# Kernel tuning notes

Hardware: AMD Instinct MI355X
Metric: run time of the kernel (lower is better)

Reference implementation:

```python
import jax, jax.numpy as jnp
import numpy as np

MARGIN = 0.3
N_CLASSES = 1024
N_SAMPLES = 32
D = 512


def setup_inputs() -> dict:
    key = jax.random.key(0)
    k1, k2 = jax.random.split(key)
    embeddings = jax.random.normal(k1, (2 * N_CLASSES * N_SAMPLES, D), dtype=jnp.float32)
    target = jax.random.randint(k2, (2 * N_CLASSES * N_SAMPLES,), 0, N_CLASSES, dtype=jnp.int64)
    return {"embeddings": embeddings, "target": target}


def reference(embeddings, target):
    # [C, 2, S, D]: per class, block 0 = positives, block 1 = negatives
    e = embeddings.reshape(N_CLASSES, 2, N_SAMPLES, D)
    pos = e[:, 0]  # [C, S, D]
    neg = e[:, 1]  # [C, S, D]
    anchor = pos.mean(axis=1, keepdims=True)  # [C, 1, D]
    ap = jnp.sum((anchor - pos) ** 2, axis=-1)  # [C, S]
    neg_d = jnp.sum((neg - anchor) ** 2, axis=-1)  # [C, S]
    # an_distances = dist(anchor, nearest negative) == min over negatives
    an = jnp.min(neg_d, axis=1, keepdims=True)  # [C, 1]
    losses = jnp.sum(jax.nn.relu(ap - an + MARGIN), axis=1)  # [C]
    return losses.mean()
```

## Files before the change

### kernel.cpp

```cpp
#include <hip/hip_runtime.h>

#define NC 1024
#define NS 32
#define DD 512
#define MARGIN 0.3f

__global__ __launch_bounds__(512) void ccl_per_class(const float* __restrict__ emb,
                                                     float* __restrict__ cls) {
    const int c = blockIdx.x;
    const int t = threadIdx.x;
    const int w = t >> 6;
    const int l = t & 63;
    const int g = l >> 4;
    const int c16 = l & 15;
    const int col4 = w * 16 + c16;
    const float4* posv = (const float4*)(emb + (size_t)c * (2 * NS * DD));
    const float4* negv = posv + NS * DD / 4;

    __shared__ float s_wap[8][4][8];
    __shared__ float s_wnd[8][4][8];

    float4 p[8], n[8];
#pragma unroll
    for (int j = 0; j < 8; ++j) p[j] = posv[(4 * j + g) * (DD / 4) + col4];
#pragma unroll
    for (int j = 0; j < 8; ++j) n[j] = negv[(4 * j + g) * (DD / 4) + col4];

    float4 a = p[0];
#pragma unroll
    for (int j = 1; j < 8; ++j) {
        a.x += p[j].x; a.y += p[j].y; a.z += p[j].z; a.w += p[j].w;
    }
    a.x += __shfl_xor(a.x, 16); a.y += __shfl_xor(a.y, 16);
    a.z += __shfl_xor(a.z, 16); a.w += __shfl_xor(a.w, 16);
    a.x += __shfl_xor(a.x, 32); a.y += __shfl_xor(a.y, 32);
    a.z += __shfl_xor(a.z, 32); a.w += __shfl_xor(a.w, 32);
    a.x *= (1.f / NS); a.y *= (1.f / NS); a.z *= (1.f / NS); a.w *= (1.f / NS);

    float apc[8], ndc[8];
#pragma unroll
    for (int j = 0; j < 8; ++j) {
        float dx = p[j].x - a.x, dy = p[j].y - a.y, dz = p[j].z - a.z, dw = p[j].w - a.w;
        apc[j] = dx * dx + dy * dy + dz * dz + dw * dw;
        dx = n[j].x - a.x; dy = n[j].y - a.y; dz = n[j].z - a.z; dw = n[j].w - a.w;
        ndc[j] = dx * dx + dy * dy + dz * dz + dw * dw;
    }

#define BSTEP(arr, m, half)                                        \
    {                                                              \
        _Pragma("unroll")                                          \
        for (int i = 0; i < (half); ++i) {                         \
            float lo = arr[i], hi = arr[i + (half)];               \
            float send = (l & (m)) ? lo : hi;                      \
            float recv = __shfl_xor(send, (m));                    \
            arr[i] = (l & (m)) ? (hi + recv) : (lo + recv);        \
        }                                                          \
    }
    BSTEP(apc, 1, 4) BSTEP(apc, 2, 2) BSTEP(apc, 4, 1)
    BSTEP(ndc, 1, 4) BSTEP(ndc, 2, 2) BSTEP(ndc, 4, 1)
#undef BSTEP
    float rap = apc[0] + __shfl_xor(apc[0], 8);
    float rnd = ndc[0] + __shfl_xor(ndc[0], 8);
    if ((l & 8) == 0) {
        const int jm = ((l & 1) << 2) | (l & 2) | ((l & 4) >> 2);
        s_wap[w][g][jm] = rap;
        s_wnd[w][g][jm] = rnd;
    }
    __syncthreads();

    if (t < NS) {
        const int sg = t & 3, sj = t >> 2;
        float ap = 0.f, nd = 0.f;
#pragma unroll
        for (int k = 0; k < 8; ++k) {
            ap += s_wap[k][sg][sj];
            nd += s_wnd[k][sg][sj];
        }
        float an = nd;
#pragma unroll
        for (int m = 1; m < 32; m <<= 1) an = fminf(an, __shfl_xor(an, m));
        float hl = fmaxf(ap - an + MARGIN, 0.f);
#pragma unroll
        for (int m = 1; m < 32; m <<= 1) hl += __shfl_xor(hl, m);
        if (t == 0) cls[c] = hl;
    }
}

__global__ __launch_bounds__(64) void ccl_reduce(const float* __restrict__ class_loss,
                                                 float* __restrict__ out) {
    const int t = threadIdx.x;
    const float4* v4 = (const float4*)class_loss;
    float4 x0 = v4[t], x1 = v4[t + 64], x2 = v4[t + 128], x3 = v4[t + 192];
    float v = (x0.x + x0.y + x0.z + x0.w) + (x1.x + x1.y + x1.z + x1.w) +
              (x2.x + x2.y + x2.z + x2.w) + (x3.x + x3.y + x3.z + x3.w);
#pragma unroll
    for (int m = 1; m < 64; m <<= 1) v += __shfl_xor(v, m);
    if (t == 0) out[0] = v * (1.f / NC);
}

extern "C" void kernel_launch(void* const* d_in, const int* in_sizes, int n_in,
                              void* d_out, int out_size, void* d_ws, size_t ws_size,
                              hipStream_t stream) {
    const float* emb = (const float*)d_in[0];
    float* cls = (float*)d_ws;
    float* out = (float*)d_out;
    ccl_per_class<<<NC, 512, 0, stream>>>(emb, cls);
    ccl_reduce<<<1, 64, 0, stream>>>(cls, out);
}
```

Baseline: 26.58 us.

## Process two classes per block with prefetch of second class during first reduction

Each block now handles two classes. It issues the loads for the second class's positives and negatives before doing the shuffle and LDS reduction of the first class. The aim is to hide global memory latency behind the reduction work and to halve the number of blocks. The cost is roughly double the vector register use per thread, which may lower occupancy, and fewer blocks (512) across the CUs.

```diff
diff --git a/kernel.cpp b/kernel.cpp
--- a/kernel.cpp
+++ b/kernel.cpp
@@ -5,26 +5,38 @@
 #define DD 512
 #define MARGIN 0.3f
 
-__global__ __launch_bounds__(512) void ccl_per_class(const float* __restrict__ emb,
+__global__ __launch_bounds__(512) void ccl_two_class(const float* __restrict__ emb,
                                                      float* __restrict__ cls) {
-    const int c = blockIdx.x;
+    const int b = blockIdx.x;
     const int t = threadIdx.x;
     const int w = t >> 6;
     const int l = t & 63;
     const int g = l >> 4;
-    const int c16 = l & 15;
-    const int col4 = w * 16 + c16;
-    const float4* posv = (const float4*)(emb + (size_t)c * (2 * NS * DD));
-    const float4* negv = posv + NS * DD / 4;
+    const int col4 = (w << 4) + (l & 15);
+    const int roff = DD / 4;
 
-    __shared__ float s_wap[8][4][8];
-    __shared__ float s_wnd[8][4][8];
+    const float4* base0 = (const float4*)(emb + (size_t)(2 * b) * (2 * NS * DD));
+    const float4* base1 = base0 + (2 * NS * DD) / 4;
+
+    __shared__ float s_ap0[8][4][8], s_nd0[8][4][8];
+    __shared__ float s_ap1[8][4][8], s_nd1[8][4][8];
+
+#define BSTEP(arr, m, half)                                        \
+    {                                                              \
+        _Pragma("unroll")                                          \
+        for (int i = 0; i < (half); ++i) {                         \
+            float lo = arr[i], hi = arr[i + (half)];               \
+            float send = (l & (m)) ? lo : hi;                      \
+            float recv = __shfl_xor(send, (m));                    \
+            arr[i] = (l & (m)) ? (hi + recv) : (lo + recv);        \
+        }                                                          \
+    }
 
     float4 p[8], n[8];
 #pragma unroll
-    for (int j = 0; j < 8; ++j) p[j] = posv[(4 * j + g) * (DD / 4) + col4];
+    for (int j = 0; j < 8; ++j) p[j] = base0[(4 * j + g) * roff + col4];
 #pragma unroll
-    for (int j = 0; j < 8; ++j) n[j] = negv[(4 * j + g) * (DD / 4) + col4];
+    for (int j = 0; j < 8; ++j) n[j] = base0[NS * roff + (4 * j + g) * roff + col4];
 
     float4 a = p[0];
 #pragma unroll
@@ -46,25 +58,69 @@
         ndc[j] = dx * dx + dy * dy + dz * dz + dw * dw;
     }
 
-#define BSTEP(arr, m, half)                                        \
-    {                                                              \
-        _Pragma("unroll")                                          \
-        for (int i = 0; i < (half); ++i) {                         \
-            float lo = arr[i], hi = arr[i + (half)];               \
-            float send = (l & (m)) ? lo : hi;                      \
-            float recv = __shfl_xor(send, (m));                    \
-            arr[i] = (l & (m)) ? (hi + recv) : (lo + recv);        \
-        }                                                          \
-    }
+    asm volatile("" ::: "memory");
+    float4 q[8], mm[8];
+#pragma unroll
+    for (int j = 0; j < 8; ++j) q[j] = base1[(4 * j + g) * roff + col4];
+#pragma unroll
+    for (int j = 0; j < 8; ++j) mm[j] = base1[NS * roff + (4 * j + g) * roff + col4];
+
     BSTEP(apc, 1, 4) BSTEP(apc, 2, 2) BSTEP(apc, 4, 1)
     BSTEP(ndc, 1, 4) BSTEP(ndc, 2, 2) BSTEP(ndc, 4, 1)
-#undef BSTEP
-    float rap = apc[0] + __shfl_xor(apc[0], 8);
-    float rnd = ndc[0] + __shfl_xor(ndc[0], 8);
-    if ((l & 8) == 0) {
-        const int jm = ((l & 1) << 2) | (l & 2) | ((l & 4) >> 2);
-        s_wap[w][g][jm] = rap;
-        s_wnd[w][g][jm] = rnd;
+    {
+        float rap = apc[0] + __shfl_xor(apc[0], 8);
+        float rnd = ndc[0] + __shfl_xor(ndc[0], 8);
+        if ((l & 8) == 0) {
+            const int jm = ((l & 1) << 2) | (l & 2) | ((l & 4) >> 2);
+            s_ap0[w][g][jm] = rap;
+            s_nd0[w][g][jm] = rnd;
+        }
+    }
+    __syncthreads();
+
+    float4 a1 = q[0];
+#pragma unroll
+    for (int j = 1; j < 8; ++j) {
+        a1.x += q[j].x; a1.y += q[j].y; a1.z += q[j].z; a1.w += q[j].w;
+    }
+    a1.x += __shfl_xor(a1.x, 16); a1.y += __shfl_xor(a1.y, 16);
+    a1.z += __shfl_xor(a1.z, 16); a1.w += __shfl_xor(a1.w, 16);
+    a1.x += __shfl_xor(a1.x, 32); a1.y += __shfl_xor(a1.y, 32);
+    a1.z += __shfl_xor(a1.z, 32); a1.w += __shfl_xor(a1.w, 32);
+    a1.x *= (1.f / NS); a1.y *= (1.f / NS); a1.z *= (1.f / NS); a1.w *= (1.f / NS);
+
+    float apd[8], nde[8];
+#pragma unroll
+    for (int j = 0; j < 8; ++j) {
+        float dx = q[j].x - a1.x, dy = q[j].y - a1.y, dz = q[j].z - a1.z, dw = q[j].w - a1.w;
+        apd[j] = dx * dx + dy * dy + dz * dz + dw * dw;
+        dx = mm[j].x - a1.x; dy = mm[j].y - a1.y; dz = mm[j].z - a1.z; dw = mm[j].w - a1.w;
+        nde[j] = dx * dx + dy * dy + dz * dz + dw * dw;
+    }
+    BSTEP(apd, 1, 4) BSTEP(apd, 2, 2) BSTEP(apd, 4, 1)
+    BSTEP(nde, 1, 4) BSTEP(nde, 2, 2) BSTEP(nde, 4, 1)
+    {
+        float rap = apd[0] + __shfl_xor(apd[0], 8);
+        float rnd = nde[0] + __shfl_xor(nde[0], 8);
+        if ((l & 8) == 0) {
+            const int jm = ((l & 1) << 2) | (l & 2) | ((l & 4) >> 2);
+            s_ap1[w][g][jm] = rap;
+            s_nd1[w][g][jm] = rnd;
+        }
+    }
+
+    if (t < NS) {
+        const int sg = t & 3, sj = t >> 2;
+        float ap = 0.f, nd = 0.f;
+#pragma unroll
+        for (int k = 0; k < 8; ++k) { ap += s_ap0[k][sg][sj]; nd += s_nd0[k][sg][sj]; }
+        float an = nd;
+#pragma unroll
+        for (int m = 1; m < 32; m <<= 1) an = fminf(an, __shfl_xor(an, m));
+        float hl = fmaxf(ap - an + MARGIN, 0.f);
+#pragma unroll
+        for (int m = 1; m < 32; m <<= 1) hl += __shfl_xor(hl, m);
+        if (t == 0) cls[2 * b] = hl;
     }
     __syncthreads();
 
@@ -72,18 +128,16 @@
         const int sg = t & 3, sj = t >> 2;
         float ap = 0.f, nd = 0.f;
 #pragma unroll
-        for (int k = 0; k < 8; ++k) {
-            ap += s_wap[k][sg][sj];
-            nd += s_wnd[k][sg][sj];
-        }
+        for (int k = 0; k < 8; ++k) { ap += s_ap1[k][sg][sj]; nd += s_nd1[k][sg][sj]; }
         float an = nd;
 #pragma unroll
         for (int m = 1; m < 32; m <<= 1) an = fminf(an, __shfl_xor(an, m));
         float hl = fmaxf(ap - an + MARGIN, 0.f);
 #pragma unroll
         for (int m = 1; m < 32; m <<= 1) hl += __shfl_xor(hl, m);
-        if (t == 0) cls[c] = hl;
+        if (t == 0) cls[2 * b + 1] = hl;
     }
+#undef BSTEP
 }
 
 __global__ __launch_bounds__(64) void ccl_reduce(const float* __restrict__ class_loss,
@@ -104,6 +158,6 @@
     const float* emb = (const float*)d_in[0];
     float* cls = (float*)d_ws;
     float* out = (float*)d_out;
-    ccl_per_class<<<NC, 512, 0, stream>>>(emb, cls);
+    ccl_two_class<<<NC / 2, 512, 0, stream>>>(emb, cls);
     ccl_reduce<<<1, 64, 0, stream>>>(cls, out);
 }
```

New measurement: 27.22 us. 1.02x slower.
